# Kernel optimization log

Measured on AMD Instinct MI355X. Metric: run time of the kernel, lower is better.

Reference implementation:

```python
import jax, jax.numpy as jnp
import numpy as np
import math

D_MODEL = 1024
NUM_HEADS = 16
D_K = D_MODEL // NUM_HEADS
SEQ_LEN = 2048
THETA = 10000.0


def _rope_tables(seq_len, d_k, theta):
    # inv_freq over even dims, angles repeated-interleaved to full d_k
    inv_freq = theta ** (-jnp.arange(0, d_k, 2, dtype=jnp.float32) / d_k)  # [d_k/2]
    pos = jnp.arange(seq_len, dtype=jnp.float32)                          # [s]
    angles = pos[:, None] * inv_freq[None, :]                             # [s, d_k/2]
    angles = jnp.repeat(angles, 2, axis=-1)                               # [s, d_k]
    return jnp.cos(angles), jnp.sin(angles)


def _rotate_half(x):
    # interleaved pairs: (x0,x1,x2,x3,...) -> (-x1,x0,-x3,x2,...)
    x_even = x[..., ::2]
    x_odd = x[..., 1::2]
    return jnp.stack([-x_odd, x_even], axis=-1).reshape(x.shape)


def _apply_rope(x, cos, sin):
    # x: [b, h, s, d_k]; cos/sin: [s, d_k]
    return x * cos + _rotate_half(x) * sin


def setup_inputs() -> dict:
    key = jax.random.key(0)
    ks = jax.random.split(key, 5)
    scale = 1.0 / math.sqrt(D_MODEL)
    X = jax.random.normal(ks[0], (2, SEQ_LEN, D_MODEL), dtype=jnp.float32)
    Wq = jax.random.normal(ks[1], (D_MODEL, D_MODEL), dtype=jnp.float32) * scale
    Wk = jax.random.normal(ks[2], (D_MODEL, D_MODEL), dtype=jnp.float32) * scale
    Wv = jax.random.normal(ks[3], (D_MODEL, D_MODEL), dtype=jnp.float32) * scale
    Wo = jax.random.normal(ks[4], (D_MODEL, D_MODEL), dtype=jnp.float32) * scale
    return {"X": X, "Wq": Wq, "Wk": Wk, "Wv": Wv, "Wo": Wo}


def reference(X, Wq, Wk, Wv, Wo):
    b, s, _ = X.shape
    h, dk = NUM_HEADS, D_K

    def proj(W):
        return (X @ W.T).reshape(b, s, h, dk).transpose(0, 2, 1, 3)  # [b,h,s,dk]

    q, k, v = proj(Wq), proj(Wk), proj(Wv)

    cos, sin = _rope_tables(s, dk, THETA)
    q = _apply_rope(q, cos, sin)
    k = _apply_rope(k, cos, sin)

    scores = jnp.einsum('bhid,bhjd->bhij', q, k) / math.sqrt(dk)
    causal = jnp.tril(jnp.ones((s, s), dtype=bool))
    scores = jnp.where(causal[None, None], scores, -jnp.inf)
    probs = jax.nn.softmax(scores, axis=-1)
    attended = jnp.einsum('bhij,bhjd->bhid', probs, v)               # [b,h,s,dk]

    out = attended.transpose(0, 2, 1, 3).reshape(b, s, h * dk)
    return out @ Wo.T
```

## Files before the change

kernel.cpp:

```cpp
#include <hip/hip_runtime.h>
#include <stdint.h>

#define D_MODEL 1024
#define NUM_HEADS 16
#define DK 64
#define SEQ 2048
#define BATCH 2
#define MROWS (BATCH * SEQ)
#define LOG2E 1.4426950408889634f
#define FIXM 14.0f

typedef short bf16x8 __attribute__((ext_vector_type(8)));
typedef float f32x4 __attribute__((ext_vector_type(4)));
typedef float f32x16 __attribute__((ext_vector_type(16)));

__device__ __forceinline__ unsigned short f2bf(float f) {
    unsigned int u = __float_as_uint(f);
    u = (u + 0x7fffu + ((u >> 16) & 1u)) >> 16;
    return (unsigned short)u;
}
__device__ __forceinline__ unsigned short f2bf_trunc(float f) {
    return (unsigned short)(__float_as_uint(f) >> 16);
}
__device__ __forceinline__ float bf2f(unsigned short h) {
    return __uint_as_float(((unsigned int)h) << 16);
}
__device__ __forceinline__ void async16(const void* g, void* l) {
    __builtin_amdgcn_global_load_lds(
        (const __attribute__((address_space(1))) void*)g,
        (__attribute__((address_space(3))) void*)l, 16, 0, 0);
}
#define SWZ64(row, b) ((((row) * 8) + ((b) ^ ((row) & 7))) * 8)

__global__ void cast_all(const float4* __restrict__ X, const float4* __restrict__ Wq,
                         const float4* __restrict__ Wk, const float4* __restrict__ Wv,
                         const float4* __restrict__ Wo, ushort4* __restrict__ Xb,
                         ushort4* __restrict__ Wqkvb, ushort4* __restrict__ Wob) {
    int i = blockIdx.x * blockDim.x + threadIdx.x;
    const float4* src;
    ushort4* dst;
    int off;
    if (i < 1048576) { src = X; dst = Xb; off = i; }
    else if (i < 1310720) { src = Wq; dst = Wqkvb; off = i - 1048576; }
    else if (i < 1572864) { src = Wk; dst = Wqkvb + 262144; off = i - 1310720; }
    else if (i < 1835008) { src = Wv; dst = Wqkvb + 524288; off = i - 1572864; }
    else { src = Wo; dst = Wob; off = i - 1835008; }
    float4 v = src[off];
    ushort4 o;
    o.x = f2bf(v.x); o.y = f2bf(v.y); o.z = f2bf(v.z); o.w = f2bf(v.w);
    dst[off] = o;
}

template <int TN, int OUT_BF16>
__global__ __launch_bounds__(256) void gemm_tile(
    const unsigned short* __restrict__ A, const unsigned short* __restrict__ B,
    void* __restrict__ Cout, int M, int N, int K) {
    __shared__ unsigned short As[128 * 64];
    __shared__ unsigned short Bs[TN * 64];
    const int m0 = blockIdx.y * 128, n0 = blockIdx.x * TN;
    const int t = threadIdx.x;
    const int lane = t & 63, wave = t >> 6;
    const int mA = lane & 15, quad = lane >> 4;
    constexpr int MI = (TN == 128) ? 4 : 2;
    constexpr int NI = 4;
    const int wr = (TN == 128) ? (wave >> 1) * 64 : wave * 32;
    const int wc = (TN == 128) ? (wave & 1) * 64 : 0;

    f32x4 acc[MI][NI] = {};
    for (int k0 = 0; k0 < K; k0 += 64) {
#pragma unroll
        for (int i = 0; i < 4; ++i) {
            int ch = i * 256 + t;
            int r = ch >> 3, b = (ch & 7) ^ (r & 7);
            async16(A + (size_t)(m0 + r) * K + k0 + b * 8, (char*)As + ch * 16);
        }
#pragma unroll
        for (int i = 0; i < TN / 32; ++i) {
            int ch = i * 256 + t;
            int r = ch >> 3, b = (ch & 7) ^ (r & 7);
            async16(B + (size_t)(n0 + r) * K + k0 + b * 8, (char*)Bs + ch * 16);
        }
        __syncthreads();
#pragma unroll
        for (int kk = 0; kk < 2; ++kk) {
            bf16x8 af[MI], bfr[NI];
#pragma unroll
            for (int mi = 0; mi < MI; ++mi) {
                int rr = wr + mi * 16 + mA;
                af[mi] = *(const bf16x8*)&As[SWZ64(rr, kk * 4 + quad)];
            }
#pragma unroll
            for (int ni = 0; ni < NI; ++ni) {
                int rr = wc + ni * 16 + mA;
                bfr[ni] = *(const bf16x8*)&Bs[SWZ64(rr, kk * 4 + quad)];
            }
#pragma unroll
            for (int mi = 0; mi < MI; ++mi)
#pragma unroll
                for (int ni = 0; ni < NI; ++ni)
                    acc[mi][ni] = __builtin_amdgcn_mfma_f32_16x16x32_bf16(
                        af[mi], bfr[ni], acc[mi][ni], 0, 0, 0);
        }
        __syncthreads();
    }
#pragma unroll
    for (int mi = 0; mi < MI; ++mi)
#pragma unroll
        for (int ni = 0; ni < NI; ++ni)
#pragma unroll
            for (int r = 0; r < 4; ++r) {
                int gm = m0 + wr + mi * 16 + quad * 4 + r;
                int gn = n0 + wc + ni * 16 + mA;
                if (OUT_BF16)
                    ((unsigned short*)Cout)[(size_t)gm * N + gn] = f2bf(acc[mi][ni][r]);
                else
                    ((float*)Cout)[(size_t)gm * N + gn] = acc[mi][ni][r];
            }
}

__global__ __launch_bounds__(256) void rope_vt(const unsigned short* __restrict__ QKV,
                                               unsigned short* __restrict__ Qr,
                                               unsigned short* __restrict__ Kr,
                                               unsigned short* __restrict__ Vt) {
    __shared__ unsigned short T[64][80];
    const int bx = blockIdx.x;
    const int t = threadIdx.x;
    if (bx < 4096) {
        int tid = bx * 256 + t;
        int bs = tid >> 8;
        int p4 = tid & 255;
        int b = bs >> 11, spos = bs & 2047;
        int h = p4 >> 4, dd = (p4 & 15) * 4;
        float sn0, cs0, sn1, cs1;
        {
            float if0 = __expf(-(float)dd * (9.210340371976184f / 64.0f));
            float if1 = __expf(-(float)(dd + 2) * (9.210340371976184f / 64.0f));
            __sincosf((float)spos * if0, &sn0, &cs0);
            __sincosf((float)spos * if1, &sn1, &cs1);
        }
        const float SCQ = 0.125f * LOG2E;
        float cs0q = cs0 * SCQ, sn0q = sn0 * SCQ;
        float cs1q = cs1 * SCQ, sn1q = sn1 * SCQ;
        size_t src = (size_t)bs * 3072 + h * 64 + dd;
        ushort4 qw = *(const ushort4*)&QKV[src];
        ushort4 kw = *(const ushort4*)&QKV[src + 1024];
        ushort4 qo_, ko_;
        float e = bf2f(qw.x), o = bf2f(qw.y);
        qo_.x = f2bf(e * cs0q - o * sn0q); qo_.y = f2bf(o * cs0q + e * sn0q);
        e = bf2f(qw.z); o = bf2f(qw.w);
        qo_.z = f2bf(e * cs1q - o * sn1q); qo_.w = f2bf(o * cs1q + e * sn1q);
        e = bf2f(kw.x); o = bf2f(kw.y);
        ko_.x = f2bf(e * cs0 - o * sn0); ko_.y = f2bf(o * cs0 + e * sn0);
        e = bf2f(kw.z); o = bf2f(kw.w);
        ko_.z = f2bf(e * cs1 - o * sn1); ko_.w = f2bf(o * cs1 + e * sn1);
        size_t qb = (((size_t)(b * NUM_HEADS + h) * SEQ + spos) * DK + dd);
        *(ushort4*)&Qr[qb] = qo_;
        *(ushort4*)&Kr[qb] = ko_;
    } else {
        int idx = bx - 4096;
        const int s0 = (idx & 31) * 64, bh = idx >> 5;
        const int b = bh >> 4, h = bh & 15;
#pragma unroll
        for (int i = 0; i < 2; ++i) {
            int ch = i * 256 + t;
            int row = ch >> 3, bc = ch & 7;
            *(int4*)&T[row][bc * 8] =
                *(const int4*)&QKV[(size_t)(b * SEQ + s0 + row) * 3072 + 2048 + h * 64 + bc * 8];
        }
        __syncthreads();
#pragma unroll
        for (int i = 0; i < 2; ++i) {
            int ch = i * 256 + t;
            int d = ch >> 3, sb = ch & 7;
            unsigned short tmp[8];
#pragma unroll
            for (int j = 0; j < 8; ++j) tmp[j] = T[sb * 8 + j][d];
            *(int4*)&Vt[(size_t)bh * DK * SEQ + (size_t)d * SEQ + s0 + sb * 8] = *(int4*)tmp;
        }
    }
}

__global__ __launch_bounds__(256, 2) void flash_attn8(
    const unsigned short* __restrict__ Qr, const unsigned short* __restrict__ Kr,
    const unsigned short* __restrict__ Vt, unsigned short* __restrict__ Att) {
    __shared__ unsigned short Ks[2][64 * 64];
    __shared__ unsigned short Vs[2][64 * 64];
    __shared__ unsigned short Ps[2][32 * 64];
    const int bh = blockIdx.x;
    const int pr = blockIdx.y;
    const int t = threadIdx.x;
    const int lane = t & 63, wave = t >> 6;
    const int l31 = lane & 31, lh = lane >> 5;
    const int wq = wave >> 1, wj = wave & 1;
    const size_t qkbase = (size_t)bh * SEQ * DK;
    const unsigned short* Kg = Kr + qkbase;
    const unsigned short* Vg = Vt + (size_t)bh * DK * SEQ;
    const int qtA = pr, qtB = 31 - pr;
    const int itA = qtA + 1, itTot = qtA + qtB + 2;
    unsigned short* PB = Ps[wq];
    const int b_ = bh >> 4, h_ = bh & 15;

    int qt = qtA;
    int qb = qt * 64 + wq * 32;

    bf16x8 aq[4];
#pragma unroll
    for (int kk = 0; kk < 4; ++kk)
        aq[kk] = *(const bf16x8*)&Qr[qkbase + (size_t)(qb + l31) * DK + kk * 16 + lh * 8];

    f32x16 accT;
#pragma unroll
    for (int r = 0; r < 16; ++r) accT[r] = 0.f;
    float lsum[16];
#pragma unroll
    for (int r = 0; r < 16; ++r) lsum[r] = 0.f;

#pragma unroll
    for (int i = 0; i < 2; ++i) {
        int ch = i * 256 + t;
        int row = ch >> 3, sb = (ch & 7) ^ (row & 7);
        async16(Kg + (size_t)row * DK + sb * 8, (char*)Ks[0] + ch * 16);
        async16(Vg + (size_t)row * SEQ + sb * 8, (char*)Vs[0] + ch * 16);
    }

    for (int it = 0; it < itTot; ++it) {
        const int jt = (it >= itA) ? it - itA : it;
        __syncthreads();
        const int cur = it & 1;
        if (it + 1 < itTot) {
            const int njt = (it + 1 >= itA) ? it + 1 - itA : it + 1;
            const int j1 = njt * 64;
#pragma unroll
            for (int i = 0; i < 2; ++i) {
                int ch = i * 256 + t;
                int row = ch >> 3, sb = (ch & 7) ^ (row & 7);
                async16(Kg + (size_t)(j1 + row) * DK + sb * 8, (char*)Ks[cur ^ 1] + ch * 16);
                async16(Vg + (size_t)row * SEQ + j1 + sb * 8, (char*)Vs[cur ^ 1] + ch * 16);
            }
        }
        const unsigned short* Kt = Ks[cur];
        const unsigned short* Vtile = Vs[cur];
        const int diag = (jt == qt);

        if (!(diag && wq == 0 && wj == 1)) {
            f32x16 sc;
#pragma unroll
            for (int r = 0; r < 16; ++r) sc[r] = 0.f;
            __builtin_amdgcn_s_setprio(1);
#pragma unroll
            for (int kk = 0; kk < 4; ++kk) {
                bf16x8 kf = *(const bf16x8*)&Kt[SWZ64(wj * 32 + l31, kk * 2 + lh)];
                sc = __builtin_amdgcn_mfma_f32_32x32x16_bf16(aq[kk], kf, sc, 0, 0, 0);
            }
            __builtin_amdgcn_s_setprio(0);
            if (diag && wj == wq) {
#pragma unroll
                for (int r = 0; r < 16; ++r) {
                    int ql = (r & 3) + 8 * (r >> 2) + 4 * lh;
                    if (l31 > ql) sc[r] = -1e30f;
                }
            }
#pragma unroll
            for (int r = 0; r < 16; ++r) {
                float p = __builtin_amdgcn_exp2f(sc[r] - FIXM);
                lsum[r] += p;
                int ql = (r & 3) + 8 * (r >> 2) + 4 * lh;
                PB[SWZ64(ql, wj * 4 + (l31 >> 3)) + (l31 & 7)] = f2bf_trunc(p);
            }
        }
        asm volatile("s_waitcnt lgkmcnt(0)" ::: "memory");
        __builtin_amdgcn_s_barrier();
        asm volatile("" ::: "memory");
        __builtin_amdgcn_sched_barrier(0);

        const int kmax = (diag && wq == 0) ? 2 : 4;
        __builtin_amdgcn_s_setprio(1);
        for (int kk = 0; kk < kmax; ++kk) {
            bf16x8 ap = *(const bf16x8*)&PB[SWZ64(l31, kk * 2 + lh)];
            bf16x8 vf = *(const bf16x8*)&Vtile[SWZ64(wj * 32 + l31, kk * 2 + lh)];
            accT = __builtin_amdgcn_mfma_f32_32x32x16_bf16(vf, ap, accT, 0, 0, 0);
        }
        __builtin_amdgcn_s_setprio(0);

        if (it == itA - 1 || it == itTot - 1) {
#pragma unroll
            for (int r = 0; r < 16; ++r)
#pragma unroll
                for (int off = 1; off < 32; off <<= 1)
                    lsum[r] += __shfl_xor(lsum[r], off, 64);
            __syncthreads();
            float* LP = (float*)Ps;
            if (l31 == 0)
#pragma unroll
                for (int r = 0; r < 16; ++r)
                    LP[(wq * 2 + wj) * 32 + (r & 3) + 8 * (r >> 2) + 4 * lh] = lsum[r];
            __syncthreads();
            const float rl = 1.0f / (LP[wq * 64 + l31] + LP[wq * 64 + 32 + l31]);
            const int qg = qb + l31;
#pragma unroll
            for (int rg = 0; rg < 4; ++rg) {
                ushort4 o;
                o.x = f2bf(accT[rg * 4 + 0] * rl);
                o.y = f2bf(accT[rg * 4 + 1] * rl);
                o.z = f2bf(accT[rg * 4 + 2] * rl);
                o.w = f2bf(accT[rg * 4 + 3] * rl);
                *(ushort4*)&Att[(size_t)(b_ * SEQ + qg) * D_MODEL + h_ * DK + wj * 32 + 8 * rg + 4 * lh] = o;
            }
            if (it == itA - 1) {
                qt = qtB;
                qb = qt * 64 + wq * 32;
#pragma unroll
                for (int kk = 0; kk < 4; ++kk)
                    aq[kk] = *(const bf16x8*)&Qr[qkbase + (size_t)(qb + l31) * DK + kk * 16 + lh * 8];
#pragma unroll
                for (int r = 0; r < 16; ++r) { accT[r] = 0.f; lsum[r] = 0.f; }
            }
        }
    }
}

extern "C" void kernel_launch(void* const* d_in, const int* in_sizes, int n_in,
                              void* d_out, int out_size, void* d_ws, size_t ws_size,
                              hipStream_t stream) {
    const float* X = (const float*)d_in[0];
    const float* Wq = (const float*)d_in[1];
    const float* Wk = (const float*)d_in[2];
    const float* Wv = (const float*)d_in[3];
    const float* Wo = (const float*)d_in[4];

    char* ws = (char*)d_ws;
    unsigned short* Xb     = (unsigned short*)(ws + 0);
    unsigned short* Wqkvb  = (unsigned short*)(ws + (8u << 20));
    unsigned short* Wob    = (unsigned short*)(ws + (14u << 20));
    unsigned short* QKVraw = (unsigned short*)(ws + (16u << 20));
    unsigned short* Kr     = (unsigned short*)(ws + (40u << 20));
    unsigned short* Vt     = (unsigned short*)(ws + (48u << 20));
    unsigned short* Qr     = Xb;
    unsigned short* Att    = QKVraw;

    cast_all<<<8192, 256, 0, stream>>>((const float4*)X, (const float4*)Wq,
                                       (const float4*)Wk, (const float4*)Wv,
                                       (const float4*)Wo, (ushort4*)Xb,
                                       (ushort4*)Wqkvb, (ushort4*)Wob);

    gemm_tile<128, 1><<<dim3(3072 / 128, MROWS / 128), 256, 0, stream>>>(
        Xb, Wqkvb, QKVraw, MROWS, 3072, D_MODEL);

    rope_vt<<<4096 + 1024, 256, 0, stream>>>(QKVraw, Qr, Kr, Vt);

    flash_attn8<<<dim3(BATCH * NUM_HEADS, 16), 256, 0, stream>>>(Qr, Kr, Vt, Att);

    gemm_tile<64, 0><<<dim3(D_MODEL / 64, MROWS / 128), 256, 0, stream>>>(
        Att, Wob, d_out, MROWS, D_MODEL, D_MODEL);
}
```

Baseline: 185.9 us.

## Keep attention probabilities in registers via permlane swap and drop LDS P staging

The flash attention kernel now computes S transposed (K as the A operand), so each wave holds the full 64-key score tile for its 32 queries. The probabilities are packed to bf16 with v_cvt_pk_bf16_f32 and rearranged with v_permlane32_swap directly into the B-operand layout of the PV MFMA. This removes the shared-memory P buffer, the mid-iteration barrier and the cross-wave row-sum reduction. Each block now handles a single query tile (grid doubled to 32 tiles, launch bounds raised to 4 blocks) instead of a paired tile for load balance. In exchange every wave recomputes QK^T for both key halves, which duplicates score work across the two d-split waves, and causal load balance now depends on the hardware scheduler.

```diff
diff --git a/kernel.cpp b/kernel.cpp
--- a/kernel.cpp
+++ b/kernel.cpp
@@ -19,9 +19,6 @@
     u = (u + 0x7fffu + ((u >> 16) & 1u)) >> 16;
     return (unsigned short)u;
 }
-__device__ __forceinline__ unsigned short f2bf_trunc(float f) {
-    return (unsigned short)(__float_as_uint(f) >> 16);
-}
 __device__ __forceinline__ float bf2f(unsigned short h) {
     return __uint_as_float(((unsigned int)h) << 16);
 }
@@ -29,6 +26,11 @@
     __builtin_amdgcn_global_load_lds(
         (const __attribute__((address_space(1))) void*)g,
         (__attribute__((address_space(3))) void*)l, 16, 0, 0);
+}
+__device__ __forceinline__ unsigned int cvtpk(float lo, float hi) {
+    unsigned int r;
+    asm("v_cvt_pk_bf16_f32 %0, %1, %2" : "=v"(r) : "v"(lo), "v"(hi));
+    return r;
 }
 #define SWZ64(row, b) ((((row) * 8) + ((b) ^ ((row) & 7))) * 8)
 
@@ -180,40 +182,31 @@
     }
 }
 
-__global__ __launch_bounds__(256, 2) void flash_attn8(
+__global__ __launch_bounds__(256, 4) void flash_attn9(
     const unsigned short* __restrict__ Qr, const unsigned short* __restrict__ Kr,
     const unsigned short* __restrict__ Vt, unsigned short* __restrict__ Att) {
     __shared__ unsigned short Ks[2][64 * 64];
     __shared__ unsigned short Vs[2][64 * 64];
-    __shared__ unsigned short Ps[2][32 * 64];
     const int bh = blockIdx.x;
-    const int pr = blockIdx.y;
+    const int qt = 31 - (int)blockIdx.y;
     const int t = threadIdx.x;
     const int lane = t & 63, wave = t >> 6;
     const int l31 = lane & 31, lh = lane >> 5;
-    const int wq = wave >> 1, wj = wave & 1;
+    const int wq = wave >> 1, wd = wave & 1;
     const size_t qkbase = (size_t)bh * SEQ * DK;
     const unsigned short* Kg = Kr + qkbase;
     const unsigned short* Vg = Vt + (size_t)bh * DK * SEQ;
-    const int qtA = pr, qtB = 31 - pr;
-    const int itA = qtA + 1, itTot = qtA + qtB + 2;
-    unsigned short* PB = Ps[wq];
-    const int b_ = bh >> 4, h_ = bh & 15;
-
-    int qt = qtA;
-    int qb = qt * 64 + wq * 32;
+    const int qg = qt * 64 + wq * 32 + l31;
 
     bf16x8 aq[4];
 #pragma unroll
     for (int kk = 0; kk < 4; ++kk)
-        aq[kk] = *(const bf16x8*)&Qr[qkbase + (size_t)(qb + l31) * DK + kk * 16 + lh * 8];
+        aq[kk] = *(const bf16x8*)&Qr[qkbase + (size_t)qg * DK + kk * 16 + lh * 8];
 
     f32x16 accT;
 #pragma unroll
     for (int r = 0; r < 16; ++r) accT[r] = 0.f;
-    float lsum[16];
-#pragma unroll
-    for (int r = 0; r < 16; ++r) lsum[r] = 0.f;
+    float la[4] = {0.f, 0.f, 0.f, 0.f};
 
 #pragma unroll
     for (int i = 0; i < 2; ++i) {
@@ -223,13 +216,11 @@
         async16(Vg + (size_t)row * SEQ + sb * 8, (char*)Vs[0] + ch * 16);
     }
 
-    for (int it = 0; it < itTot; ++it) {
-        const int jt = (it >= itA) ? it - itA : it;
+    for (int jt = 0; jt <= qt; ++jt) {
         __syncthreads();
-        const int cur = it & 1;
-        if (it + 1 < itTot) {
-            const int njt = (it + 1 >= itA) ? it + 1 - itA : it + 1;
-            const int j1 = njt * 64;
+        const int cur = jt & 1;
+        if (jt < qt) {
+            const int j1 = (jt + 1) * 64;
 #pragma unroll
             for (int i = 0; i < 2; ++i) {
                 int ch = i * 256 + t;
@@ -240,82 +231,111 @@
         }
         const unsigned short* Kt = Ks[cur];
         const unsigned short* Vtile = Vs[cur];
-        const int diag = (jt == qt);
-
-        if (!(diag && wq == 0 && wj == 1)) {
-            f32x16 sc;
-#pragma unroll
-            for (int r = 0; r < 16; ++r) sc[r] = 0.f;
-            __builtin_amdgcn_s_setprio(1);
-#pragma unroll
-            for (int kk = 0; kk < 4; ++kk) {
-                bf16x8 kf = *(const bf16x8*)&Kt[SWZ64(wj * 32 + l31, kk * 2 + lh)];
-                sc = __builtin_amdgcn_mfma_f32_32x32x16_bf16(aq[kk], kf, sc, 0, 0, 0);
-            }
-            __builtin_amdgcn_s_setprio(0);
-            if (diag && wj == wq) {
+        const bool diag = (jt == qt);
+        const bool do1 = !(diag && wq == 0);
+
+        f32x16 s0, s1;
+#pragma unroll
+        for (int r = 0; r < 16; ++r) { s0[r] = 0.f; s1[r] = 0.f; }
+        __builtin_amdgcn_s_setprio(1);
+#pragma unroll
+        for (int kk = 0; kk < 4; ++kk) {
+            bf16x8 kf0 = *(const bf16x8*)&Kt[SWZ64(l31, kk * 2 + lh)];
+            s0 = __builtin_amdgcn_mfma_f32_32x32x16_bf16(kf0, aq[kk], s0, 0, 0, 0);
+            if (do1) {
+                bf16x8 kf1 = *(const bf16x8*)&Kt[SWZ64(32 + l31, kk * 2 + lh)];
+                s1 = __builtin_amdgcn_mfma_f32_32x32x16_bf16(kf1, aq[kk], s1, 0, 0, 0);
+            }
+        }
+        __builtin_amdgcn_s_setprio(0);
+        if (diag) {
+            if (wq == 0) {
 #pragma unroll
                 for (int r = 0; r < 16; ++r) {
-                    int ql = (r & 3) + 8 * (r >> 2) + 4 * lh;
-                    if (l31 > ql) sc[r] = -1e30f;
+                    int crow = (r & 3) + 8 * (r >> 2) + 4 * lh;
+                    if (crow > l31) s0[r] = -1e30f;
                 }
-            }
+            } else {
+#pragma unroll
+                for (int r = 0; r < 16; ++r) {
+                    int crow = (r & 3) + 8 * (r >> 2) + 4 * lh;
+                    if (crow > l31) s1[r] = -1e30f;
+                }
+            }
+        }
+
+#pragma unroll
+        for (int r = 0; r < 16; ++r) {
+            s0[r] = __builtin_amdgcn_exp2f(s0[r] - FIXM);
+            la[r & 3] += s0[r];
+        }
+        if (do1) {
 #pragma unroll
             for (int r = 0; r < 16; ++r) {
-                float p = __builtin_amdgcn_exp2f(sc[r] - FIXM);
-                lsum[r] += p;
-                int ql = (r & 3) + 8 * (r >> 2) + 4 * lh;
-                PB[SWZ64(ql, wj * 4 + (l31 >> 3)) + (l31 & 7)] = f2bf_trunc(p);
-            }
-        }
-        asm volatile("s_waitcnt lgkmcnt(0)" ::: "memory");
-        __builtin_amdgcn_s_barrier();
-        asm volatile("" ::: "memory");
-        __builtin_amdgcn_sched_barrier(0);
-
-        const int kmax = (diag && wq == 0) ? 2 : 4;
+                s1[r] = __builtin_amdgcn_exp2f(s1[r] - FIXM);
+                la[r & 3] += s1[r];
+            }
+        }
+
+        bf16x8 fr[4];
+        {
+            unsigned int u0 = cvtpk(s0[0], s0[1]), v0 = cvtpk(s0[4], s0[5]);
+            unsigned int u1 = cvtpk(s0[2], s0[3]), v1 = cvtpk(s0[6], s0[7]);
+            asm("v_permlane32_swap_b32 %0, %1" : "+v"(u0), "+v"(v0));
+            asm("v_permlane32_swap_b32 %0, %1" : "+v"(u1), "+v"(v1));
+            uint4 w = {u0, u1, v0, v1};
+            fr[0] = *(bf16x8*)&w;
+            unsigned int u2 = cvtpk(s0[8], s0[9]), v2 = cvtpk(s0[12], s0[13]);
+            unsigned int u3 = cvtpk(s0[10], s0[11]), v3 = cvtpk(s0[14], s0[15]);
+            asm("v_permlane32_swap_b32 %0, %1" : "+v"(u2), "+v"(v2));
+            asm("v_permlane32_swap_b32 %0, %1" : "+v"(u3), "+v"(v3));
+            uint4 w2_ = {u2, u3, v2, v3};
+            fr[1] = *(bf16x8*)&w2_;
+        }
+        if (do1) {
+            unsigned int u0 = cvtpk(s1[0], s1[1]), v0 = cvtpk(s1[4], s1[5]);
+            unsigned int u1 = cvtpk(s1[2], s1[3]), v1 = cvtpk(s1[6], s1[7]);
+            asm("v_permlane32_swap_b32 %0, %1" : "+v"(u0), "+v"(v0));
+            asm("v_permlane32_swap_b32 %0, %1" : "+v"(u1), "+v"(v1));
+            uint4 w = {u0, u1, v0, v1};
+            fr[2] = *(bf16x8*)&w;
+            unsigned int u2 = cvtpk(s1[8], s1[9]), v2 = cvtpk(s1[12], s1[13]);
+            unsigned int u3 = cvtpk(s1[10], s1[11]), v3 = cvtpk(s1[14], s1[15]);
+            asm("v_permlane32_swap_b32 %0, %1" : "+v"(u2), "+v"(v2));
+            asm("v_permlane32_swap_b32 %0, %1" : "+v"(u3), "+v"(v3));
+            uint4 w2_ = {u2, u3, v2, v3};
+            fr[3] = *(bf16x8*)&w2_;
+        }
+
         __builtin_amdgcn_s_setprio(1);
-        for (int kk = 0; kk < kmax; ++kk) {
-            bf16x8 ap = *(const bf16x8*)&PB[SWZ64(l31, kk * 2 + lh)];
-            bf16x8 vf = *(const bf16x8*)&Vtile[SWZ64(wj * 32 + l31, kk * 2 + lh)];
-            accT = __builtin_amdgcn_mfma_f32_32x32x16_bf16(vf, ap, accT, 0, 0, 0);
+#pragma unroll
+        for (int kk = 0; kk < 2; ++kk) {
+            bf16x8 vf = *(const bf16x8*)&Vtile[SWZ64(wd * 32 + l31, kk * 2 + lh)];
+            accT = __builtin_amdgcn_mfma_f32_32x32x16_bf16(vf, fr[kk], accT, 0, 0, 0);
+        }
+        if (do1) {
+#pragma unroll
+            for (int kk = 2; kk < 4; ++kk) {
+                bf16x8 vf = *(const bf16x8*)&Vtile[SWZ64(wd * 32 + l31, kk * 2 + lh)];
+                accT = __builtin_amdgcn_mfma_f32_32x32x16_bf16(vf, fr[kk], accT, 0, 0, 0);
+            }
         }
         __builtin_amdgcn_s_setprio(0);
-
-        if (it == itA - 1 || it == itTot - 1) {
-#pragma unroll
-            for (int r = 0; r < 16; ++r)
-#pragma unroll
-                for (int off = 1; off < 32; off <<= 1)
-                    lsum[r] += __shfl_xor(lsum[r], off, 64);
-            __syncthreads();
-            float* LP = (float*)Ps;
-            if (l31 == 0)
-#pragma unroll
-                for (int r = 0; r < 16; ++r)
-                    LP[(wq * 2 + wj) * 32 + (r & 3) + 8 * (r >> 2) + 4 * lh] = lsum[r];
-            __syncthreads();
-            const float rl = 1.0f / (LP[wq * 64 + l31] + LP[wq * 64 + 32 + l31]);
-            const int qg = qb + l31;
-#pragma unroll
-            for (int rg = 0; rg < 4; ++rg) {
-                ushort4 o;
-                o.x = f2bf(accT[rg * 4 + 0] * rl);
-                o.y = f2bf(accT[rg * 4 + 1] * rl);
-                o.z = f2bf(accT[rg * 4 + 2] * rl);
-                o.w = f2bf(accT[rg * 4 + 3] * rl);
-                *(ushort4*)&Att[(size_t)(b_ * SEQ + qg) * D_MODEL + h_ * DK + wj * 32 + 8 * rg + 4 * lh] = o;
-            }
-            if (it == itA - 1) {
-                qt = qtB;
-                qb = qt * 64 + wq * 32;
-#pragma unroll
-                for (int kk = 0; kk < 4; ++kk)
-                    aq[kk] = *(const bf16x8*)&Qr[qkbase + (size_t)(qb + l31) * DK + kk * 16 + lh * 8];
-#pragma unroll
-                for (int r = 0; r < 16; ++r) { accT[r] = 0.f; lsum[r] = 0.f; }
-            }
-        }
+    }
+
+    float lt = (la[0] + la[1]) + (la[2] + la[3]);
+    lt += __shfl_xor(lt, 32, 64);
+    const float rl = 1.0f / lt;
+
+    const int b_ = bh >> 4, h_ = bh & 15;
+#pragma unroll
+    for (int rg = 0; rg < 4; ++rg) {
+        ushort4 o;
+        o.x = f2bf(accT[rg * 4 + 0] * rl);
+        o.y = f2bf(accT[rg * 4 + 1] * rl);
+        o.z = f2bf(accT[rg * 4 + 2] * rl);
+        o.w = f2bf(accT[rg * 4 + 3] * rl);
+        *(ushort4*)&Att[(size_t)(b_ * SEQ + qg) * D_MODEL + h_ * DK + wd * 32 + 8 * rg + 4 * lh] = o;
     }
 }
 
@@ -348,7 +368,7 @@
 
     rope_vt<<<4096 + 1024, 256, 0, stream>>>(QKVraw, Qr, Kr, Vt);
 
-    flash_attn8<<<dim3(BATCH * NUM_HEADS, 16), 256, 0, stream>>>(Qr, Kr, Vt, Att);
+    flash_attn9<<<dim3(BATCH * NUM_HEADS, 32), 256, 0, stream>>>(Qr, Kr, Vt, Att);
 
     gemm_tile<64, 0><<<dim3(D_MODEL / 64, MROWS / 128), 256, 0, stream>>>(
         Att, Wob, d_out, MROWS, D_MODEL, D_MODEL);
```

Measured after the change: 186.2 us. About the same (+0.2%).
